# Performance work log

Measured on AMD Instinct MI355X. Metric: run time of the kernel, lower is better.

The kernel has to match this reference:

```python
import jax, jax.numpy as jnp
import numpy as np

DIM = 192
WS = 8        # window_size
NH = 6        # num_heads
SHIFT = 4     # shift_size
HD = DIM // NH


def setup_inputs() -> dict:
    key = jax.random.key(0)
    ks = jax.random.split(key, 5)
    return {
        'x': jax.random.normal(ks[0], (4, DIM, 256, 256), dtype=jnp.float32),
        'qkv_w': jax.random.normal(ks[1], (DIM, 3 * DIM), dtype=jnp.float32) * 0.02,
        'qkv_b': jax.random.normal(ks[2], (3 * DIM,), dtype=jnp.float32) * 0.02,
        'proj_w': jax.random.normal(ks[3], (DIM, DIM), dtype=jnp.float32) * 0.02,
        'proj_b': jax.random.normal(ks[4], (DIM,), dtype=jnp.float32) * 0.02,
    }


def _forward(x, qkv_w, qkv_b, proj_w, proj_b):
    b, c, h, w = x.shape
    pad_h = (WS - h % WS) % WS
    pad_w = (WS - w % WS) % WS
    x = jnp.transpose(x, (0, 2, 3, 1))  # b,h,w,c
    if pad_h or pad_w:
        x = jnp.pad(x, ((0, 0), (0, pad_h), (0, pad_w), (0, 0)))
    hp, wp = h + pad_h, w + pad_w
    if SHIFT > 0:
        x = jnp.roll(x, shift=(-SHIFT, -SHIFT), axis=(1, 2))
    # window partition -> (nW, WS*WS, c)
    x = x.reshape(b, hp // WS, WS, wp // WS, WS, c)
    x = jnp.transpose(x, (0, 1, 3, 2, 4, 5)).reshape(-1, WS * WS, c)
    # qkv projection
    qkv = x @ qkv_w + qkv_b                       # (nW, T, 3c)
    q, k, v = jnp.split(qkv, 3, axis=-1)
    nw, t = x.shape[0], WS * WS
    q = q.reshape(nw, t, NH, HD)
    k = k.reshape(nw, t, NH, HD)
    v = v.reshape(nw, t, NH, HD)
    scale = 1.0 / np.sqrt(HD).astype(np.float32)
    attn = jnp.einsum('nqhd,nkhd->nhqk', q, k) * scale
    attn = jax.nn.softmax(attn, axis=-1)
    out = jnp.einsum('nhqk,nkhd->nqhd', attn, v).reshape(nw, t, c)
    out = out @ proj_w + proj_b
    # window reverse -> (b, hp, wp, c)
    out = out.reshape(b, hp // WS, wp // WS, WS, WS, c)
    out = jnp.transpose(out, (0, 1, 3, 2, 4, 5)).reshape(b, hp, wp, c)
    if SHIFT > 0:
        out = jnp.roll(out, shift=(SHIFT, SHIFT), axis=(1, 2))
    if pad_h or pad_w:
        out = out[:, :h, :w, :]
    return jnp.transpose(out, (0, 3, 1, 2))


def reference(x, qkv_w, qkv_b, proj_w, proj_b):
    return _forward(x, qkv_w, qkv_b, proj_w, proj_b)
```

## Files before the change

kernel.cpp:

```cpp
#include <hip/hip_runtime.h>

typedef _Float16 half8 __attribute__((ext_vector_type(8)));
typedef _Float16 half4v __attribute__((ext_vector_type(4)));
typedef _Float16 half2v __attribute__((ext_vector_type(2)));
typedef float floatx4 __attribute__((ext_vector_type(4)));

namespace {
constexpr int RES = 256;
constexpr float SCALE_ = 0.17677669529663687f;
constexpr int QPK_HALFS = 36 * 6 * 64 * 8;
constexpr int PPK_HALFS = 12 * 6 * 64 * 8;
constexpr size_t WT_BYTES = (QPK_HALFS + PPK_HALFS) * 2;
constexpr size_t NPX = 131072;
constexpr size_t QK_BYTES = NPX * 384 * 2;
constexpr size_t V_BYTES  = NPX * 192 * 2;
}

__global__ void prep_pack(const float* __restrict__ qkv_w,
                          const float* __restrict__ proj_w,
                          _Float16* __restrict__ qpk,
                          _Float16* __restrict__ ppk) {
  const int idx = blockIdx.x * 256 + threadIdx.x;
  const float* W;
  _Float16* dst;
  int ncol, base;
  if (idx < 13824) {
    W = qkv_w; dst = qpk; ncol = 576; base = idx;
  } else {
    W = proj_w; dst = ppk; ncol = 192; base = idx - 13824;
  }
  const int lane = base & 63;
  const int kk = (base >> 6) % 6;
  const int nt = base / 384;
  const int col = nt * 16 + (lane & 15);
  const int krow = kk * 32 + (lane >> 4) * 8;
  half8 v;
#pragma unroll
  for (int e = 0; e < 8; ++e) v[e] = (_Float16)W[(size_t)(krow + e) * ncol + col];
  *(half8*)(dst + (size_t)base * 8) = v;
}

__global__ __launch_bounds__(512, 4)
void qkv_gemm(const float* __restrict__ x, const _Float16* __restrict__ qpk,
              const float* __restrict__ qkv_b, _Float16* __restrict__ qk,
              _Float16* __restrict__ vpl, const int b_off) {
  __shared__ _Float16 pool[26112];
  const int pid = blockIdx.x;
  const int w0 = (pid & 1) * 128;
  const int h = (pid >> 1) & (RES - 1);
  const int bb = pid >> 9;
  const int tid = threadIdx.x;

#pragma unroll
  for (int t = 0; t < 6; ++t) {
    const int idx = tid + t * 512;
    const int w4 = idx & 31;
    const int c2 = idx >> 5;
    const size_t base =
        (((size_t)(b_off + bb) * 192 + c2 * 2) * RES + h) * RES + w0 + w4 * 4;
    const float4 va = *reinterpret_cast<const float4*>(x + base);
    const float4 vb = *reinterpret_cast<const float4*>(x + base + (size_t)RES * RES);
    half2v p;
    p[0] = (_Float16)va.x; p[1] = (_Float16)vb.x;
    *(half2v*)&pool[(w4 * 4 + 0) * 200 + c2 * 2] = p;
    p[0] = (_Float16)va.y; p[1] = (_Float16)vb.y;
    *(half2v*)&pool[(w4 * 4 + 1) * 200 + c2 * 2] = p;
    p[0] = (_Float16)va.z; p[1] = (_Float16)vb.z;
    *(half2v*)&pool[(w4 * 4 + 2) * 200 + c2 * 2] = p;
    p[0] = (_Float16)va.w; p[1] = (_Float16)vb.w;
    *(half2v*)&pool[(w4 * 4 + 3) * 200 + c2 * 2] = p;
  }
  __syncthreads();

  const int wv = tid >> 6, lane = tid & 63;
  const int ln = lane & 15, quad = lane >> 4;
  const int mp = wv >> 1, hf = wv & 1;

  half8 af[2][6];
#pragma unroll
  for (int mm = 0; mm < 2; ++mm)
#pragma unroll
    for (int k = 0; k < 6; ++k)
      af[mm][k] =
          *(const half8*)&pool[(mp * 32 + mm * 16 + ln) * 200 + k * 32 + quad * 8];
  __syncthreads();

  const int rh = (h + RES - 4) & (RES - 1);
  const int rowbase = (bb * RES + rh) * RES;

  for (int cc = 0; cc < 3; ++cc) {
#pragma unroll
    for (int i = 0; i < 6; ++i) {
      const int ntl = hf * 6 + i;
      const int ntg = cc * 12 + ntl;
      const _Float16* bp = qpk + (size_t)ntg * 3072 + lane * 8;
      floatx4 acc0 = {0.f, 0.f, 0.f, 0.f};
      floatx4 acc1 = {0.f, 0.f, 0.f, 0.f};
#pragma unroll
      for (int k = 0; k < 6; ++k) {
        const half8 bf = *(const half8*)(bp + k * 512);
        acc0 = __builtin_amdgcn_mfma_f32_16x16x32_f16(af[0][k], bf, acc0, 0, 0, 0);
        acc1 = __builtin_amdgcn_mfma_f32_16x16x32_f16(af[1][k], bf, acc1, 0, 0, 0);
      }
      const float bias = qkv_b[cc * 192 + ntl * 16 + ln];
      const float scl = (cc == 0) ? SCALE_ : 1.0f;
      const int tok0 = mp * 32 + quad * 4;
      if (cc < 2) {
#pragma unroll
        for (int j = 0; j < 4; ++j) {
          pool[(tok0 + j) * 200 + ntl * 16 + ln] =
              (_Float16)((acc0[j] + bias) * scl);
          pool[(tok0 + 16 + j) * 200 + ntl * 16 + ln] =
              (_Float16)((acc1[j] + bias) * scl);
        }
      } else {
        half4v p0, p1;
#pragma unroll
        for (int j = 0; j < 4; ++j) {
          p0[j] = (_Float16)(acc0[j] + bias);
          p1[j] = (_Float16)(acc1[j] + bias);
        }
        *(half4v*)&pool[(ntl * 16 + ln) * 132 + tok0] = p0;
        *(half4v*)&pool[(ntl * 16 + ln) * 132 + tok0 + 16] = p1;
      }
    }
    __syncthreads();
    if (cc < 2) {
#pragma unroll
      for (int p = 0; p < 6; ++p) {
        const int idx = tid + p * 512;
        const int px = idx / 24, off = idx - px * 24;
        const half8 v = *(const half8*)&pool[px * 200 + off * 8];
        const int rw = (w0 + px + RES - 4) & (RES - 1);
        *(half8*)&qk[(size_t)(rowbase + rw) * 384 + cc * 192 + off * 8] = v;
      }
    } else {
#pragma unroll
      for (int p = 0; p < 12; ++p) {
        const int idx = tid + p * 512;
        const int d = idx >> 5, g4 = idx & 31;
        const half4v v = *(const half4v*)&pool[d * 132 + g4 * 4];
        const int rw = (w0 + g4 * 4 + RES - 4) & (RES - 1);
        *(half4v*)&vpl[(size_t)d * NPX + rowbase + rw] = v;
      }
    }
    __syncthreads();
  }
}

__global__ __launch_bounds__(384, 3)
void attn_proj(const _Float16* __restrict__ qk, const _Float16* __restrict__ vpl,
               const _Float16* __restrict__ ppk, const float* __restrict__ proj_b,
               float* __restrict__ out, const int b_off) {
  __shared__ _Float16 os_[64][200];
  __shared__ float lsx[6][1056];
  const int bid = blockIdx.x;
  const int wid = (bid & 7) * 256 + (bid >> 3);
  const int bb = wid >> 10, wh = (wid >> 5) & 31, ww = wid & 31;
  const int wv = threadIdx.x >> 6, lane = threadIdx.x & 63;
  const int ln = lane & 15, quad = lane >> 4;
  const int hd = wv;
  const int base = (bb * RES + wh * 8) * RES + ww * 8;
  float* ls = lsx[wv];
  _Float16* slab = (_Float16*)ls;

  const int p0 = base + (ln >> 3) * RES + (ln & 7);
  const _Float16* qp = qk + (size_t)p0 * 384 + hd * 32 + quad * 8;
  half8 qf[4], kf[4];
#pragma unroll
  for (int s = 0; s < 4; ++s) {
    qf[s] = *(const half8*)(qp + (size_t)s * (512 * 384));
    kf[s] = *(const half8*)(qp + (size_t)s * (512 * 384) + 192);
  }
  half8 bv[2][2];
#pragma unroll
  for (int pnt = 0; pnt < 2; ++pnt)
#pragma unroll
    for (int ks = 0; ks < 2; ++ks)
      bv[pnt][ks] = *(const half8*)(vpl +
          (size_t)(hd * 32 + pnt * 16 + ln) * NPX + base + (ks * 4 + quad) * RES);

#pragma unroll
  for (int qt = 0; qt < 4; ++qt) {
    floatx4 sc[4];
#pragma unroll
    for (int kt = 0; kt < 4; ++kt) {
      floatx4 z = {0.f, 0.f, 0.f, 0.f};
      sc[kt] = __builtin_amdgcn_mfma_f32_16x16x32_f16(kf[kt], qf[qt], z, 0, 0, 0);
    }
    float m = -3.0e38f;
#pragma unroll
    for (int kt = 0; kt < 4; ++kt)
#pragma unroll
      for (int j = 0; j < 4; ++j) m = fmaxf(m, sc[kt][j]);
    m = fmaxf(m, __shfl_xor(m, 16));
    m = fmaxf(m, __shfl_xor(m, 32));
    float sum = 0.f;
    float pe[4][4];
#pragma unroll
    for (int kt = 0; kt < 4; ++kt)
#pragma unroll
      for (int j = 0; j < 4; ++j) {
        pe[kt][j] = __expf(sc[kt][j] - m);
        sum += pe[kt][j];
      }
    sum += __shfl_xor(sum, 16);
    sum += __shfl_xor(sum, 32);
    const float inv = 1.0f / sum;
#pragma unroll
    for (int kt = 0; kt < 4; ++kt) {
      half4v h4;
#pragma unroll
      for (int j = 0; j < 4; ++j) h4[j] = (_Float16)(pe[kt][j] * inv);
      *(half4v*)&slab[ln * 72 + kt * 16 + quad * 4] = h4;
    }
    const half8 pa0 = *(const half8*)&slab[ln * 72 + quad * 8];
    const half8 pa1 = *(const half8*)&slab[ln * 72 + 32 + quad * 8];
    floatx4 aO0 = {0.f, 0.f, 0.f, 0.f};
    floatx4 aO1 = {0.f, 0.f, 0.f, 0.f};
    aO0 = __builtin_amdgcn_mfma_f32_16x16x32_f16(pa0, bv[0][0], aO0, 0, 0, 0);
    aO0 = __builtin_amdgcn_mfma_f32_16x16x32_f16(pa1, bv[0][1], aO0, 0, 0, 0);
    aO1 = __builtin_amdgcn_mfma_f32_16x16x32_f16(pa0, bv[1][0], aO1, 0, 0, 0);
    aO1 = __builtin_amdgcn_mfma_f32_16x16x32_f16(pa1, bv[1][1], aO1, 0, 0, 0);
#pragma unroll
    for (int j = 0; j < 4; ++j) {
      os_[qt * 16 + quad * 4 + j][hd * 32 + ln] = (_Float16)aO0[j];
      os_[qt * 16 + quad * 4 + j][hd * 32 + 16 + ln] = (_Float16)aO1[j];
    }
  }
  __syncthreads();

  const int b = b_off + bb;
#pragma unroll
  for (int t = 0; t < 2; ++t) {
    const int nt = wv + t * 6;
    const _Float16* bp = ppk + (size_t)nt * 3072 + lane * 8;
    const float bias = proj_b[nt * 16 + ln];
#pragma unroll
    for (int mt = 0; mt < 4; ++mt) {
      floatx4 acc = {0.f, 0.f, 0.f, 0.f};
#pragma unroll
      for (int k = 0; k < 6; ++k) {
        const half8 a = *(const half8*)&os_[mt * 16 + ln][k * 32 + quad * 8];
        const half8 bf = *(const half8*)(bp + k * 512);
        acc = __builtin_amdgcn_mfma_f32_16x16x32_f16(a, bf, acc, 0, 0, 0);
      }
#pragma unroll
      for (int j = 0; j < 4; ++j)
        ls[ln * 66 + mt * 16 + quad * 4 + j] = acc[j] + bias;
    }
#pragma unroll
    for (int s = 0; s < 8; ++s) {
      const int rid = s * 16 + (lane >> 2);
      const int cl = rid >> 3, r = rid & 7;
      const int cw = (lane & 3) * 2;
      const float2 v = *(const float2*)&ls[cl * 66 + r * 8 + cw];
      const int h2 = (wh * 8 + 4 + r) & (RES - 1);
      const int w2 = (ww * 8 + 4 + cw) & (RES - 1);
      *reinterpret_cast<float2*>(
          out + (((size_t)b * 192 + nt * 16 + cl) * RES + h2) * RES + w2) = v;
    }
  }
}

__global__ __launch_bounds__(512, 6)
void win_attn_fused(const float* __restrict__ x,
                    const _Float16* __restrict__ qpk,
                    const float* __restrict__ qkv_b,
                    const _Float16* __restrict__ ppk,
                    const float* __restrict__ proj_b,
                    float* __restrict__ out) {
  __shared__ _Float16 xs[64][200];
  __shared__ _Float16 qB[64][40];
  __shared__ _Float16 kB[64][40];
  __shared__ _Float16 vT[32][72];
  __shared__ _Float16 st[64][80];
  __shared__ float rowred[64];

  const int wid = ((int)blockIdx.x & 7) * 512 + ((int)blockIdx.x >> 3);
  const int b = wid >> 10, wh = (wid >> 5) & 31, ww = wid & 31;
  const int wv = threadIdx.x >> 6;
  const int lane = threadIdx.x & 63;
  const int ln = lane & 15;
  const int quad = lane >> 4;
  const int mt = wv >> 1, ng = wv & 1;

#pragma unroll
  for (int t = 0; t < 3; ++t) {
    const int f = threadIdx.x + t * 512;
    const int c2 = (f & 31) + 32 * (f >> 9);
    const int tg = (f >> 5) & 15;
    const int r = tg >> 1;
    const int cw = (tg & 1) * 4;
    const int h = (wh * 8 + r + 4) & (RES - 1);
    const int w0 = (ww * 8 + cw + 4) & (RES - 1);
    const size_t base = (((size_t)b * 192 + c2 * 2) * RES + h) * RES + w0;
    const float4 va = *reinterpret_cast<const float4*>(x + base);
    const float4 vb = *reinterpret_cast<const float4*>(x + base + (size_t)RES * RES);
    const int tok = tg * 4;
    half2v p;
    p[0] = (_Float16)va.x; p[1] = (_Float16)vb.x;
    *(half2v*)&xs[tok + 0][c2 * 2] = p;
    p[0] = (_Float16)va.y; p[1] = (_Float16)vb.y;
    *(half2v*)&xs[tok + 1][c2 * 2] = p;
    p[0] = (_Float16)va.z; p[1] = (_Float16)vb.z;
    *(half2v*)&xs[tok + 2][c2 * 2] = p;
    p[0] = (_Float16)va.w; p[1] = (_Float16)vb.w;
    *(half2v*)&xs[tok + 3][c2 * 2] = p;
  }
  __syncthreads();

  floatx4 acc6[6];
#pragma unroll
  for (int i = 0; i < 6; ++i) acc6[i] = (floatx4){0.f, 0.f, 0.f, 0.f};

  for (int hd = 0; hd < 6; ++hd) {
    {
      int colb[3];
#pragma unroll
      for (int i = 0; i < 3; ++i) {
        const int nt = ng * 3 + i;
        colb[i] = (nt >> 1) * 192 + hd * 32 + (nt & 1) * 16;
      }
      floatx4 acc[3];
#pragma unroll
      for (int i = 0; i < 3; ++i) acc[i] = (floatx4){0.f, 0.f, 0.f, 0.f};
#pragma unroll
      for (int k = 0; k < 6; ++k) {
        const half8 af = *(const half8*)&xs[mt * 16 + ln][k * 32 + quad * 8];
#pragma unroll
        for (int i = 0; i < 3; ++i) {
          const half8 bf = *(const half8*)(qpk +
              (size_t)(colb[i] >> 4) * 3072 + k * 512 + lane * 8);
          acc[i] = __builtin_amdgcn_mfma_f32_16x16x32_f16(af, bf, acc[i], 0, 0, 0);
        }
      }
#pragma unroll
      for (int i = 0; i < 3; ++i) {
        const int nt = ng * 3 + i;
        const int sec = nt >> 1;
        const float bias = qkv_b[colb[i] + ln];
        const int tok0 = mt * 16 + quad * 4;
        const int d = (nt & 1) * 16 + ln;
        if (sec == 0) {
#pragma unroll
          for (int j = 0; j < 4; ++j)
            qB[tok0 + j][d] = (_Float16)((acc[i][j] + bias) * SCALE_);
        } else if (sec == 1) {
#pragma unroll
          for (int j = 0; j < 4; ++j)
            kB[tok0 + j][d] = (_Float16)(acc[i][j] + bias);
        } else {
#pragma unroll
          for (int j = 0; j < 4; ++j)
            vT[d][tok0 + j] = (_Float16)(acc[i][j] + bias);
        }
      }
    }
    __syncthreads();

#pragma unroll
    for (int i = 0; i < 2; ++i) {
      const int t = wv * 2 + i;
      const int smt = t >> 2, snt = t & 3;
      const half8 aq = *(const half8*)&qB[smt * 16 + ln][quad * 8];
      const half8 bk = *(const half8*)&kB[snt * 16 + ln][quad * 8];
      floatx4 acc = {0.f, 0.f, 0.f, 0.f};
      acc = __builtin_amdgcn_mfma_f32_16x16x32_f16(aq, bk, acc, 0, 0, 0);
      const int r0 = smt * 16 + quad * 4;
#pragma unroll
      for (int j = 0; j < 4; ++j)
        st[r0 + j][snt * 16 + ln] = (_Float16)acc[j];
    }
    __syncthreads();

    {
      const int row = threadIdx.x >> 3;
      const int sl = threadIdx.x & 7;
      const half8 hv = *(const half8*)&st[row][sl * 8];
      float m = -3.0e38f;
#pragma unroll
      for (int j = 0; j < 8; ++j) m = fmaxf(m, (float)hv[j]);
      m = fmaxf(m, __shfl_xor(m, 1));
      m = fmaxf(m, __shfl_xor(m, 2));
      m = fmaxf(m, __shfl_xor(m, 4));
      float s = 0.f;
      half8 ev;
#pragma unroll
      for (int j = 0; j < 8; ++j) {
        const float e = __expf((float)hv[j] - m);
        s += e;
        ev[j] = (_Float16)e;
      }
      *(half8*)&st[row][sl * 8] = ev;
      s += __shfl_xor(s, 1);
      s += __shfl_xor(s, 2);
      s += __shfl_xor(s, 4);
      if (sl == 0) rowred[row] = 1.0f / s;
    }
    __syncthreads();

    {
      const int pmt = wv >> 1, pnt = wv & 1;
      floatx4 acc = {0.f, 0.f, 0.f, 0.f};
#pragma unroll
      for (int ks = 0; ks < 2; ++ks) {
        const half8 ap = *(const half8*)&st[pmt * 16 + ln][ks * 32 + quad * 8];
        const half8 bvv = *(const half8*)&vT[pnt * 16 + ln][ks * 32 + quad * 8];
        acc = __builtin_amdgcn_mfma_f32_16x16x32_f16(ap, bvv, acc, 0, 0, 0);
      }
      const int tok0 = pmt * 16 + quad * 4;
      const int d = pnt * 16 + ln;
#pragma unroll
      for (int j = 0; j < 4; ++j)
        qB[tok0 + j][d] = (_Float16)(acc[j] * rowred[tok0 + j]);
    }
    __syncthreads();

    {
      const half8 af = *(const half8*)&qB[mt * 16 + ln][quad * 8];
#pragma unroll
      for (int i = 0; i < 6; ++i) {
        const int nt = ng * 6 + i;
        const half8 bf = *(const half8*)(ppk +
            (size_t)nt * 3072 + hd * 512 + lane * 8);
        acc6[i] = __builtin_amdgcn_mfma_f32_16x16x32_f16(af, bf, acc6[i], 0, 0, 0);
      }
    }
    __syncthreads();
  }

  {
#pragma unroll
    for (int i = 0; i < 6; ++i) {
      const int c = (ng * 6 + i) * 16 + ln;
      const float bias = proj_b[c];
      const int tok0 = mt * 16 + quad * 4;
      const int r = tok0 >> 3, cw = tok0 & 7;
      const int h = (wh * 8 + r + 4) & (RES - 1);
      const int w0 = (ww * 8 + cw + 4) & (RES - 1);
      float4 vv;
      vv.x = acc6[i][0] + bias;
      vv.y = acc6[i][1] + bias;
      vv.z = acc6[i][2] + bias;
      vv.w = acc6[i][3] + bias;
      *reinterpret_cast<float4*>(
          out + (((size_t)b * 192 + c) * RES + h) * RES + w0) = vv;
    }
  }
}

extern "C" void kernel_launch(void* const* d_in, const int* in_sizes, int n_in,
                              void* d_out, int out_size, void* d_ws, size_t ws_size,
                              hipStream_t stream) {
  (void)in_sizes; (void)n_in; (void)out_size;
  const float* x      = (const float*)d_in[0];
  const float* qkv_w  = (const float*)d_in[1];
  const float* qkv_b  = (const float*)d_in[2];
  const float* proj_w = (const float*)d_in[3];
  const float* proj_b = (const float*)d_in[4];
  float* out = (float*)d_out;

  _Float16* qpk = (_Float16*)d_ws;
  _Float16* ppk = qpk + QPK_HALFS;

  prep_pack<<<72, 256, 0, stream>>>(qkv_w, proj_w, qpk, ppk);

  if (ws_size >= WT_BYTES + QK_BYTES + V_BYTES) {
    _Float16* qk  = (_Float16*)((char*)d_ws + WT_BYTES);
    _Float16* vpl = (_Float16*)((char*)d_ws + WT_BYTES + QK_BYTES);
    for (int c = 0; c < 2; ++c) {
      const int b_off = c * 2;
      qkv_gemm<<<1024, 512, 0, stream>>>(x, qpk, qkv_b, qk, vpl, b_off);
      attn_proj<<<2048, 384, 0, stream>>>(qk, vpl, ppk, proj_b, out, b_off);
    }
  } else {
    win_attn_fused<<<4096, 512, 0, stream>>>(x, qpk, qkv_b, ppk, proj_b, out);
  }
}
```

Baseline: 625.7 us.

## Store V in window-blocked layout and process all batches in one launch pair

V is now written in a per-window blocked layout ([row][window col][dim][8 px]), so the attention kernel reads each V fragment as one contiguous 16-byte chunk instead of loading strided planes spaced NPX apart. The V staging pad in shared memory changes from 132 to 136, and the store loop now walks dimension-fastest. When the workspace is large enough, the host runs all four batches in a single qkv_gemm/attn_proj pair instead of two chunks, cutting launch count and giving the GPU larger grids. The cost is a larger workspace requirement and more intermediate data live at once, which may reduce L2/MALL reuse between the two kernels.

Result: slower. 644.2 us (+2.9%).

```diff
diff --git a/kernel.cpp b/kernel.cpp
--- a/kernel.cpp
+++ b/kernel.cpp
@@ -11,9 +11,8 @@
 constexpr int QPK_HALFS = 36 * 6 * 64 * 8;
 constexpr int PPK_HALFS = 12 * 6 * 64 * 8;
 constexpr size_t WT_BYTES = (QPK_HALFS + PPK_HALFS) * 2;
-constexpr size_t NPX = 131072;
-constexpr size_t QK_BYTES = NPX * 384 * 2;
-constexpr size_t V_BYTES  = NPX * 192 * 2;
+constexpr size_t QKB1 = (size_t)65536 * 384 * 2;
+constexpr size_t V1 = (size_t)65536 * 192 * 2;
 }
 
 __global__ void prep_pack(const float* __restrict__ qkv_w,
@@ -43,7 +42,7 @@
 __global__ __launch_bounds__(512, 4)
 void qkv_gemm(const float* __restrict__ x, const _Float16* __restrict__ qpk,
               const float* __restrict__ qkv_b, _Float16* __restrict__ qk,
-              _Float16* __restrict__ vpl, const int b_off) {
+              _Float16* __restrict__ v2, const int b_off) {
   __shared__ _Float16 pool[26112];
   const int pid = blockIdx.x;
   const int w0 = (pid & 1) * 128;
@@ -87,6 +86,7 @@
 
   const int rh = (h + RES - 4) & (RES - 1);
   const int rowbase = (bb * RES + rh) * RES;
+  const int vrow = bb * RES + rh;
 
   for (int cc = 0; cc < 3; ++cc) {
 #pragma unroll
@@ -120,8 +120,9 @@
           p0[j] = (_Float16)(acc0[j] + bias);
           p1[j] = (_Float16)(acc1[j] + bias);
         }
-        *(half4v*)&pool[(ntl * 16 + ln) * 132 + tok0] = p0;
-        *(half4v*)&pool[(ntl * 16 + ln) * 132 + tok0 + 16] = p1;
+        const int d = ntl * 16 + ln;
+        *(half4v*)&pool[d * 136 + tok0] = p0;
+        *(half4v*)&pool[d * 136 + tok0 + 16] = p1;
       }
     }
     __syncthreads();
@@ -138,10 +139,12 @@
 #pragma unroll
       for (int p = 0; p < 12; ++p) {
         const int idx = tid + p * 512;
-        const int d = idx >> 5, g4 = idx & 31;
-        const half4v v = *(const half4v*)&pool[d * 132 + g4 * 4];
-        const int rw = (w0 + g4 * 4 + RES - 4) & (RES - 1);
-        *(half4v*)&vpl[(size_t)d * NPX + rowbase + rw] = v;
+        const int g = idx / 192;
+        const int dd = idx - g * 192;
+        const half4v v = *(const half4v*)&pool[dd * 136 + g * 4];
+        const int rw = (w0 + g * 4 + RES - 4) & (RES - 1);
+        const int ww = rw >> 3, off = rw & 7;
+        *(half4v*)&v2[(size_t)((vrow * 32 + ww) * 192 + dd) * 8 + off] = v;
       }
     }
     __syncthreads();
@@ -149,13 +152,14 @@
 }
 
 __global__ __launch_bounds__(384, 3)
-void attn_proj(const _Float16* __restrict__ qk, const _Float16* __restrict__ vpl,
+void attn_proj(const _Float16* __restrict__ qk, const _Float16* __restrict__ v2,
                const _Float16* __restrict__ ppk, const float* __restrict__ proj_b,
                float* __restrict__ out, const int b_off) {
   __shared__ _Float16 os_[64][200];
   __shared__ float lsx[6][1056];
   const int bid = blockIdx.x;
-  const int wid = (bid & 7) * 256 + (bid >> 3);
+  const int cpx = gridDim.x >> 3;
+  const int wid = (bid & 7) * cpx + (bid >> 3);
   const int bb = wid >> 10, wh = (wid >> 5) & 31, ww = wid & 31;
   const int wv = threadIdx.x >> 6, lane = threadIdx.x & 63;
   const int ln = lane & 15, quad = lane >> 4;
@@ -176,9 +180,11 @@
 #pragma unroll
   for (int pnt = 0; pnt < 2; ++pnt)
 #pragma unroll
-    for (int ks = 0; ks < 2; ++ks)
-      bv[pnt][ks] = *(const half8*)(vpl +
-          (size_t)(hd * 32 + pnt * 16 + ln) * NPX + base + (ks * 4 + quad) * RES);
+    for (int ks = 0; ks < 2; ++ks) {
+      const int vrow = bb * RES + wh * 8 + ks * 4 + quad;
+      bv[pnt][ks] = *(const half8*)(v2 +
+          (size_t)((vrow * 32 + ww) * 192 + hd * 32 + pnt * 16 + ln) * 8);
+    }
 
 #pragma unroll
   for (int qt = 0; qt < 4; ++qt) {
@@ -466,13 +472,17 @@
 
   prep_pack<<<72, 256, 0, stream>>>(qkv_w, proj_w, qpk, ppk);
 
-  if (ws_size >= WT_BYTES + QK_BYTES + V_BYTES) {
-    _Float16* qk  = (_Float16*)((char*)d_ws + WT_BYTES);
-    _Float16* vpl = (_Float16*)((char*)d_ws + WT_BYTES + QK_BYTES);
-    for (int c = 0; c < 2; ++c) {
-      const int b_off = c * 2;
-      qkv_gemm<<<1024, 512, 0, stream>>>(x, qpk, qkv_b, qk, vpl, b_off);
-      attn_proj<<<2048, 384, 0, stream>>>(qk, vpl, ppk, proj_b, out, b_off);
+  int nb = 0;
+  if (ws_size >= WT_BYTES + 4 * (QKB1 + V1)) nb = 4;
+  else if (ws_size >= WT_BYTES + 2 * (QKB1 + V1)) nb = 2;
+
+  if (nb) {
+    _Float16* qk = (_Float16*)((char*)d_ws + WT_BYTES);
+    _Float16* v2 = (_Float16*)((char*)d_ws + WT_BYTES + (size_t)nb * QKB1);
+    for (int c = 0; c < 4 / nb; ++c) {
+      const int b_off = c * nb;
+      qkv_gemm<<<nb * 512, 512, 0, stream>>>(x, qpk, qkv_b, qk, v2, b_off);
+      attn_proj<<<nb * 1024, 384, 0, stream>>>(qk, v2, ppk, proj_b, out, b_off);
     }
   } else {
     win_attn_fused<<<4096, 512, 0, stream>>>(x, qpk, qkv_b, ppk, proj_b, out);
```
